# Kernel tuning notes

Measured on AMD Instinct MI355X. Metric: run time of the kernel, lower is better.

Reference implementation:

```python
import jax, jax.numpy as jnp
import numpy as np

H = 8          # num_heads
L = 256        # lifting_dim
DH = L // H    # head dim


def setup_inputs() -> dict:
    key = jax.random.key(0)
    ks = jax.random.split(key, 32)
    B, N, E = 4, 16384, 65536
    Dn, De, Dg = 128, 64, 32

    def lin_w(k, din, dout):
        return jax.random.normal(k, (din, dout), jnp.float32) * (din ** -0.5)

    inp = {
        "node_features": jax.random.normal(ks[0], (B, N, Dn), jnp.float32),
        "edge_features": jax.random.normal(ks[1], (B, E, De), jnp.float32),
        "energy": jax.random.normal(ks[2], (Dg,), jnp.float32),
        "W_node": lin_w(ks[3], Dn, L), "b_node": jnp.zeros((L,), jnp.float32),
        "W_edge": lin_w(ks[4], De, L), "b_edge": jnp.zeros((L,), jnp.float32),
        "W_graph": lin_w(ks[5], Dg, L), "b_graph": jnp.zeros((L,), jnp.float32),
        "Wq": lin_w(ks[6], L, L), "bq": jnp.zeros((L,), jnp.float32),
        # stacked per-hetero-type key/value projections: [3, L, L]
        "Wk": jnp.stack([lin_w(ks[7 + i], L, L) for i in range(3)]),
        "bk": jnp.zeros((3, L), jnp.float32),
        "Wv": jnp.stack([lin_w(ks[10 + i], L, L) for i in range(3)]),
        "bv": jnp.zeros((3, L), jnp.float32),
        "W_out": lin_w(ks[13], L, L), "b_out": jnp.zeros((L,), jnp.float32),
    }
    return inp


def _heads(x, B, T):
    # [B,T,L] -> [B,H,T,DH]
    return x.reshape(B, T, H, DH).transpose(0, 2, 1, 3)


def reference(node_features, edge_features, energy,
              W_node, b_node, W_edge, b_edge, W_graph, b_graph,
              Wq, bq, Wk, bk, Wv, bv, W_out, b_out):
    B, N, _ = node_features.shape
    lifted_nodes = node_features @ W_node + b_node            # [B,N,L]
    lifted_edges = edge_features @ W_edge + b_edge            # [B,E,L]
    lifted_graph = jnp.broadcast_to(energy, (B, 1, energy.shape[0])) @ W_graph + b_graph  # [B,1,L]

    hetero = [lifted_nodes, lifted_edges, lifted_graph]

    q = _heads(lifted_nodes @ Wq + bq, B, N)                  # [B,H,N,DH]
    q = jax.nn.softmax(q, axis=-1)

    out = None
    # NOTE: faithful to the original, `out` is overwritten each iteration,
    # so only the last hetero feature (graph) determines the output.
    for i in range(3):
        h = hetero[i]
        T = h.shape[1]
        k = jax.nn.softmax(_heads(h @ Wk[i] + bk[i], B, T), axis=-1)  # [B,H,T,DH]
        v = _heads(h @ Wv[i] + bv[i], B, T)                           # [B,H,T,DH]
        k_sum = k.sum(axis=-2, keepdims=True)                          # [B,H,1,DH]
        d_inv = 1.0 / jnp.clip((q * k_sum).sum(axis=-1, keepdims=True), 1e-8)  # [B,H,N,1]
        kv = jnp.einsum("bhtd,bhte->bhde", k, v)                       # [B,H,DH,DH]
        out = q + jnp.einsum("bhnd,bhde->bhne", q, kv) * d_inv         # [B,H,N,DH]

    out = out.transpose(0, 2, 1, 3).reshape(B, N, L)
    return out @ W_out + b_out
```

## Files before the change

kernel.cpp:

```cpp
#include <hip/hip_runtime.h>
#include <hip/hip_bf16.h>
#include <cstdint>
#include <cstddef>


typedef __attribute__((ext_vector_type(8))) short short8;
typedef __attribute__((ext_vector_type(4))) float floatx4;

using bf16 = __hip_bfloat16;

static constexpr int Mrows = 65536;
static constexpr int Lcols = 256;

static __device__ __forceinline__ short f2bs(float x) {
  bf16 h = __float2bfloat16(x);
  return *reinterpret_cast<short*>(&h);
}

__global__ void k_setup(const float* __restrict__ W_node,
                        const float* __restrict__ Wq,
                        const float* __restrict__ W_out,
                        const float* __restrict__ energy,
                        const float* __restrict__ W_graph,
                        const float* __restrict__ b_graph,
                        const float* __restrict__ Wk,
                        const float* __restrict__ bk,
                        const float* __restrict__ Wv,
                        const float* __restrict__ bv,
                        const float* __restrict__ b_node,
                        const float* __restrict__ bq,
                        short* __restrict__ wnq_t,
                        short* __restrict__ wto_t,
                        float* __restrict__ vvec,
                        float* __restrict__ bnq) {
  const int b = blockIdx.x;
  const int t = threadIdx.x;

  if (b < 256) {
    __shared__ float wqc[256];
    const int j = b;
    wqc[t] = Wq[t * 256 + j];
    __syncthreads();
    if (t < 128) {
      const float* wr = W_node + t * 256;
      float acc = 0.f;
#pragma unroll 8
      for (int l = 0; l < 256; ++l) acc += wr[l] * wqc[l];
      wnq_t[j * 128 + t] = f2bs(acc);
    }
  } else if (b < 512) {
    const int r = b - 256;
    wto_t[t * 256 + r] = f2bs(W_out[r * 256 + t]);
  } else {
    __shared__ float ev[32];
    __shared__ float lg[256];
    __shared__ float r1[256], r2[256];
    const int h = b - 512;
    if (t < 32) ev[t] = energy[t];
    __syncthreads();

    {
      float lgd = b_graph[t];
#pragma unroll
      for (int e = 0; e < 32; ++e) lgd += ev[e] * W_graph[e * 256 + t];
      lg[t] = lgd;
    }
    __syncthreads();

    const int g = t >> 5;
    const int c = t & 31;
    const int j = h * 32 + c;
    float p1 = 0.f, p2 = 0.f;
#pragma unroll
    for (int i = 0; i < 32; ++i) {
      const int d = g * 32 + i;
      p1 += lg[d] * Wv[2 * 65536 + d * 256 + j];
      p2 += b_node[d] * Wq[d * 256 + j];
    }
    r1[t] = p1; r2[t] = p2;
    __syncthreads();
    if (t < 32) {
      float s1 = 0.f, s2 = 0.f;
#pragma unroll
      for (int gg = 0; gg < 8; ++gg) {
        s1 += r1[gg * 32 + c]; s2 += r2[gg * 32 + c];
      }
      vvec[j] = s1 + bv[512 + j];
      bnq[j]  = s2 + bq[j];
    }
  }
}

__global__ __launch_bounds__(256, 4)
void k_fused(const float* __restrict__ nf,
             const short* __restrict__ wnq,
             const short* __restrict__ wto,
             const float* __restrict__ bnq,
             const float* __restrict__ vvec,
             const float* __restrict__ b_out,
             float* __restrict__ out) {
  constexpr int AS_STR = 136;
  constexpr int PS_STR = 264;
  constexpr int FO_STR = 260;
  __shared__ short smem[64 * PS_STR];
  float* fsm = (float*)smem;

  const int t = threadIdx.x;
  const int lane = t & 63;
  const int l15 = lane & 15;
  const int lhi = lane >> 4;
  const int cw = (t >> 6) * 64;
  const int rowBase = blockIdx.x * 64;

  {
    const int row = t >> 2;
    const int c0 = (t & 3) << 5;
    const float* src = nf + (size_t)(rowBase + row) * 128 + c0;
    short tmp[32];
#pragma unroll
    for (int i = 0; i < 8; ++i) {
      float4 f = *(const float4*)(src + i * 4);
      tmp[i * 4 + 0] = f2bs(f.x); tmp[i * 4 + 1] = f2bs(f.y);
      tmp[i * 4 + 2] = f2bs(f.z); tmp[i * 4 + 3] = f2bs(f.w);
    }
#pragma unroll
    for (int i = 0; i < 4; ++i)
      *(short8*)(&smem[row * AS_STR + c0 + i * 8]) = *(short8*)(&tmp[i * 8]);
  }
  __syncthreads();

  floatx4 acc[4][4];
#pragma unroll
  for (int m = 0; m < 4; ++m)
#pragma unroll
    for (int n = 0; n < 4; ++n) acc[m][n] = (floatx4){0.f, 0.f, 0.f, 0.f};

  {
    const short* wb = wnq + (cw + l15) * 128 + lhi * 8;
#pragma unroll
    for (int kc = 0; kc < 4; ++kc) {
      short8 af[4], bfv[4];
#pragma unroll
      for (int n = 0; n < 4; ++n)
        bfv[n] = *(const short8*)(wb + n * 16 * 128 + kc * 32);
#pragma unroll
      for (int m = 0; m < 4; ++m)
        af[m] = *(const short8*)(&smem[(m * 16 + l15) * AS_STR + kc * 32 + lhi * 8]);
#pragma unroll
      for (int m = 0; m < 4; ++m)
#pragma unroll
        for (int n = 0; n < 4; ++n)
          acc[m][n] = __builtin_amdgcn_mfma_f32_16x16x32_bf16(af[m], bfv[n],
                                                              acc[m][n], 0, 0, 0);
    }
  }
  __syncthreads();

#pragma unroll
  for (int tt = 0; tt < 2; ++tt) {
    const int col0 = cw + tt * 32 + l15;
    const int col1 = col0 + 16;
    const float b0 = bnq[col0], b1 = bnq[col1];
    const float v0v = vvec[col0], v1v = vvec[col1];
#pragma unroll
    for (int m = 0; m < 4; ++m) {
      const int row0 = m * 16 + lhi * 4;
#pragma unroll
      for (int r = 0; r < 4; ++r) {
        float e0 = __expf(acc[m][2 * tt][r] + b0);
        float e1 = __expf(acc[m][2 * tt + 1][r] + b1);
        float s = e0 + e1;
#pragma unroll
        for (int msk = 1; msk <= 8; msk <<= 1) s += __shfl_xor(s, msk);
        float inv = 1.0f / s;
        smem[(row0 + r) * PS_STR + col0] = f2bs(e0 * inv + v0v);
        smem[(row0 + r) * PS_STR + col1] = f2bs(e1 * inv + v1v);
      }
    }
  }
#pragma unroll
  for (int m = 0; m < 4; ++m)
#pragma unroll
    for (int n = 0; n < 4; ++n) acc[m][n] = (floatx4){0.f, 0.f, 0.f, 0.f};
  __syncthreads();

  {
    const short* wb = wto + (cw + l15) * 256 + lhi * 8;
#pragma unroll
    for (int kc = 0; kc < 8; ++kc) {
      short8 af[4], bfv[4];
#pragma unroll
      for (int n = 0; n < 4; ++n)
        bfv[n] = *(const short8*)(wb + n * 16 * 256 + kc * 32);
#pragma unroll
      for (int m = 0; m < 4; ++m)
        af[m] = *(const short8*)(&smem[(m * 16 + l15) * PS_STR + kc * 32 + lhi * 8]);
#pragma unroll
      for (int m = 0; m < 4; ++m)
#pragma unroll
        for (int n = 0; n < 4; ++n)
          acc[m][n] = __builtin_amdgcn_mfma_f32_16x16x32_bf16(af[m], bfv[n],
                                                              acc[m][n], 0, 0, 0);
    }
  }

  float bb[4];
#pragma unroll
  for (int n = 0; n < 4; ++n) bb[n] = b_out[cw + n * 16 + l15];

#pragma unroll
  for (int c = 0; c < 2; ++c) {
    __syncthreads();
#pragma unroll
    for (int mm = 0; mm < 2; ++mm) {
      const int m = c * 2 + mm;
#pragma unroll
      for (int n = 0; n < 4; ++n) {
        const int col = cw + n * 16 + l15;
        const int row0 = mm * 16 + lhi * 4;
#pragma unroll
        for (int r = 0; r < 4; ++r)
          fsm[(row0 + r) * FO_STR + col] = acc[m][n][r] + bb[n];
      }
    }
    __syncthreads();
#pragma unroll
    for (int i = 0; i < 8; ++i) {
      const int f = i * 256 + t;
      const int row = f >> 6;
      const int c4 = (f & 63) << 2;
      float4 vv = *(const float4*)(&fsm[row * FO_STR + c4]);
      *(float4*)(&out[(size_t)(rowBase + c * 32 + row) * Lcols + c4]) = vv;
    }
  }
}

extern "C" void kernel_launch(void* const* d_in, const int* in_sizes, int n_in,
                              void* d_out, int out_size, void* d_ws, size_t ws_size,
                              hipStream_t stream) {
  const float* node_features = (const float*)d_in[0];
  const float* energy  = (const float*)d_in[2];
  const float* W_node  = (const float*)d_in[3];
  const float* b_node  = (const float*)d_in[4];
  const float* W_graph = (const float*)d_in[7];
  const float* b_graph = (const float*)d_in[8];
  const float* Wq      = (const float*)d_in[9];
  const float* bq      = (const float*)d_in[10];
  const float* Wk      = (const float*)d_in[11];
  const float* bk      = (const float*)d_in[12];
  const float* Wv      = (const float*)d_in[13];
  const float* bv      = (const float*)d_in[14];
  const float* W_out   = (const float*)d_in[15];
  const float* b_out   = (const float*)d_in[16];

  char* ws = (char*)d_ws;
  short* wnq_t = (short*)(ws);
  short* wto_t = (short*)(ws + 65536);
  float* vvec  = (float*)(ws + 196608);
  float* bnq   = (float*)(ws + 197632);

  k_setup<<<dim3(520), dim3(256), 0, stream>>>(
      W_node, Wq, W_out, energy, W_graph, b_graph, Wk, bk, Wv, bv,
      b_node, bq, wnq_t, wto_t, vvec, bnq);

  k_fused<<<dim3(Mrows / 64), dim3(256), 0, stream>>>(
      node_features, wnq_t, wto_t, bnq, vvec, b_out, (float*)d_out);
}
```

Measured before the change: 192.6 us.

## Swap MFMA operands to get row-contiguous outputs and drop LDS output staging

Result: no change. 193.2 us (+0.3%).

```diff
diff --git a/kernel.cpp b/kernel.cpp
--- a/kernel.cpp
+++ b/kernel.cpp
@@ -5,6 +5,7 @@
 
 
 typedef __attribute__((ext_vector_type(8))) short short8;
+typedef __attribute__((ext_vector_type(4))) short short4v;
 typedef __attribute__((ext_vector_type(4))) float floatx4;
 
 using bf16 = __hip_bfloat16;
@@ -101,9 +102,7 @@
              float* __restrict__ out) {
   constexpr int AS_STR = 136;
   constexpr int PS_STR = 264;
-  constexpr int FO_STR = 260;
   __shared__ short smem[64 * PS_STR];
-  float* fsm = (float*)smem;
 
   const int t = threadIdx.x;
   const int lane = t & 63;
@@ -111,6 +110,7 @@
   const int lhi = lane >> 4;
   const int cw = (t >> 6) * 64;
   const int rowBase = blockIdx.x * 64;
+  const int colq = cw + lhi * 4;
 
   {
     const int row = t >> 2;
@@ -127,6 +127,18 @@
     for (int i = 0; i < 4; ++i)
       *(short8*)(&smem[row * AS_STR + c0 + i * 8]) = *(short8*)(&tmp[i * 8]);
   }
+
+  const short* wb1 = wnq + (cw + l15) * 128 + lhi * 8;
+  short8 pbf1[4];
+#pragma unroll
+  for (int n = 0; n < 4; ++n) pbf1[n] = *(const short8*)(wb1 + n * 16 * 128);
+  floatx4 bnq4[4], vv4[4];
+#pragma unroll
+  for (int n = 0; n < 4; ++n) {
+    bnq4[n] = *(const floatx4*)(&bnq[colq + n * 16]);
+    vv4[n]  = *(const floatx4*)(&vvec[colq + n * 16]);
+  }
+
   __syncthreads();
 
   floatx4 acc[4][4];
@@ -136,13 +148,13 @@
     for (int n = 0; n < 4; ++n) acc[m][n] = (floatx4){0.f, 0.f, 0.f, 0.f};
 
   {
-    const short* wb = wnq + (cw + l15) * 128 + lhi * 8;
 #pragma unroll
     for (int kc = 0; kc < 4; ++kc) {
       short8 af[4], bfv[4];
 #pragma unroll
       for (int n = 0; n < 4; ++n)
-        bfv[n] = *(const short8*)(wb + n * 16 * 128 + kc * 32);
+        bfv[n] = (kc == 0) ? pbf1[n]
+                           : *(const short8*)(wb1 + n * 16 * 128 + kc * 32);
 #pragma unroll
       for (int m = 0; m < 4; ++m)
         af[m] = *(const short8*)(&smem[(m * 16 + l15) * AS_STR + kc * 32 + lhi * 8]);
@@ -150,32 +162,43 @@
       for (int m = 0; m < 4; ++m)
 #pragma unroll
         for (int n = 0; n < 4; ++n)
-          acc[m][n] = __builtin_amdgcn_mfma_f32_16x16x32_bf16(af[m], bfv[n],
+          acc[m][n] = __builtin_amdgcn_mfma_f32_16x16x32_bf16(bfv[n], af[m],
                                                               acc[m][n], 0, 0, 0);
     }
   }
+
+  const short* wb2 = wto + (cw + l15) * 256 + lhi * 8;
+  short8 pbf2[4];
+#pragma unroll
+  for (int n = 0; n < 4; ++n) pbf2[n] = *(const short8*)(wb2 + n * 16 * 256);
+
   __syncthreads();
 
 #pragma unroll
-  for (int tt = 0; tt < 2; ++tt) {
-    const int col0 = cw + tt * 32 + l15;
-    const int col1 = col0 + 16;
-    const float b0 = bnq[col0], b1 = bnq[col1];
-    const float v0v = vvec[col0], v1v = vvec[col1];
-#pragma unroll
-    for (int m = 0; m < 4; ++m) {
-      const int row0 = m * 16 + lhi * 4;
+  for (int m = 0; m < 4; ++m) {
+#pragma unroll
+    for (int tt = 0; tt < 2; ++tt) {
+      const int n0 = 2 * tt, n1 = n0 + 1;
+      float e0[4], e1[4];
 #pragma unroll
       for (int r = 0; r < 4; ++r) {
-        float e0 = __expf(acc[m][2 * tt][r] + b0);
-        float e1 = __expf(acc[m][2 * tt + 1][r] + b1);
-        float s = e0 + e1;
-#pragma unroll
-        for (int msk = 1; msk <= 8; msk <<= 1) s += __shfl_xor(s, msk);
-        float inv = 1.0f / s;
-        smem[(row0 + r) * PS_STR + col0] = f2bs(e0 * inv + v0v);
-        smem[(row0 + r) * PS_STR + col1] = f2bs(e1 * inv + v1v);
+        e0[r] = __expf(acc[m][n0][r] + bnq4[n0][r]);
+        e1[r] = __expf(acc[m][n1][r] + bnq4[n1][r]);
       }
+      float s = ((e0[0] + e0[1]) + (e0[2] + e0[3]))
+              + ((e1[0] + e1[1]) + (e1[2] + e1[3]));
+      s += __shfl_xor(s, 16);
+      s += __shfl_xor(s, 32);
+      const float inv = 1.0f / s;
+      short4v p0, p1;
+#pragma unroll
+      for (int r = 0; r < 4; ++r) {
+        p0[r] = f2bs(e0[r] * inv + vv4[n0][r]);
+        p1[r] = f2bs(e1[r] * inv + vv4[n1][r]);
+      }
+      const int prow = (m * 16 + l15) * PS_STR;
+      *(short4v*)(&smem[prow + colq + n0 * 16]) = p0;
+      *(short4v*)(&smem[prow + colq + n1 * 16]) = p1;
     }
   }
 #pragma unroll
@@ -185,13 +208,13 @@
   __syncthreads();
 
   {
-    const short* wb = wto + (cw + l15) * 256 + lhi * 8;
 #pragma unroll
     for (int kc = 0; kc < 8; ++kc) {
       short8 af[4], bfv[4];
 #pragma unroll
       for (int n = 0; n < 4; ++n)
-        bfv[n] = *(const short8*)(wb + n * 16 * 256 + kc * 32);
+        bfv[n] = (kc == 0) ? pbf2[n]
+                           : *(const short8*)(wb2 + n * 16 * 256 + kc * 32);
 #pragma unroll
       for (int m = 0; m < 4; ++m)
         af[m] = *(const short8*)(&smem[(m * 16 + l15) * PS_STR + kc * 32 + lhi * 8]);
@@ -199,38 +222,22 @@
       for (int m = 0; m < 4; ++m)
 #pragma unroll
         for (int n = 0; n < 4; ++n)
-          acc[m][n] = __builtin_amdgcn_mfma_f32_16x16x32_bf16(af[m], bfv[n],
+          acc[m][n] = __builtin_amdgcn_mfma_f32_16x16x32_bf16(bfv[n], af[m],
                                                               acc[m][n], 0, 0, 0);
     }
   }
 
-  float bb[4];
-#pragma unroll
-  for (int n = 0; n < 4; ++n) bb[n] = b_out[cw + n * 16 + l15];
-
-#pragma unroll
-  for (int c = 0; c < 2; ++c) {
-    __syncthreads();
-#pragma unroll
-    for (int mm = 0; mm < 2; ++mm) {
-      const int m = c * 2 + mm;
-#pragma unroll
-      for (int n = 0; n < 4; ++n) {
-        const int col = cw + n * 16 + l15;
-        const int row0 = mm * 16 + lhi * 4;
-#pragma unroll
-        for (int r = 0; r < 4; ++r)
-          fsm[(row0 + r) * FO_STR + col] = acc[m][n][r] + bb[n];
-      }
-    }
-    __syncthreads();
-#pragma unroll
-    for (int i = 0; i < 8; ++i) {
-      const int f = i * 256 + t;
-      const int row = f >> 6;
-      const int c4 = (f & 63) << 2;
-      float4 vv = *(const float4*)(&fsm[row * FO_STR + c4]);
-      *(float4*)(&out[(size_t)(rowBase + c * 32 + row) * Lcols + c4]) = vv;
+  floatx4 bo4[4];
+#pragma unroll
+  for (int n = 0; n < 4; ++n) bo4[n] = *(const floatx4*)(&b_out[colq + n * 16]);
+
+#pragma unroll
+  for (int m = 0; m < 4; ++m) {
+    const size_t rbase = (size_t)(rowBase + m * 16 + l15) * Lcols;
+#pragma unroll
+    for (int n = 0; n < 4; ++n) {
+      floatx4 v = acc[m][n] + bo4[n];
+      *(floatx4*)(&out[rbase + colq + n * 16]) = v;
     }
   }
 }
```
